# Kernel tuning notes

Measured on AMD Instinct MI355X. Metric: run time of the kernel, lower is better.

Reference implementation:

```python
import jax, jax.numpy as jnp
import numpy as np

B, S, E, H = 4, 2048, 256, 8  # batch, seq_len, embed_dim, depth (heads)


def setup_inputs() -> dict:
    key = jax.random.key(0)
    k_x, k_q, k_k, k_v = jax.random.split(key, 4)
    return {
        "x": jax.random.normal(k_x, (B, S, E), dtype=jnp.float32),
        "w_q": jax.random.normal(k_q, (H, E, E), dtype=jnp.float32),
        "w_k": jax.random.normal(k_k, (H, E, E), dtype=jnp.float32),
        "w_v": jax.random.normal(k_v, (H, E, E), dtype=jnp.float32),
    }


def reference(x, w_q, w_k, w_v):
    # Each head uses full embed_dim projections; heads are averaged at the end.
    embed_dim = x.shape[-1]
    scale = 1.0 / np.sqrt(embed_dim).astype(np.float32)
    q = jnp.einsum("bse,hef->bhsf", x, w_q)  # [B,H,S,E]
    k = jnp.einsum("bse,hef->bhsf", x, w_k)
    v = jnp.einsum("bse,hef->bhsf", x, w_v)
    scores = jax.nn.softmax(jnp.einsum("bhsf,bhtf->bhst", q, k) * scale, axis=-1)
    out = jnp.einsum("bhst,bhtf->bhsf", scores, v)  # [B,H,S,E]
    return out.mean(axis=1)  # [B,S,E]
```

## Files before the change

### kernel.cpp

```cpp
#include <hip/hip_runtime.h>
#include <hip/hip_bf16.h>
#include <cstdint>

#define B_N 4
#define S_N 2048
#define E_N 256
#define H_N 8

typedef float f32x4 __attribute__((ext_vector_type(4)));
typedef int i32x4 __attribute__((ext_vector_type(4)));
typedef short s16x8 __attribute__((ext_vector_type(8)));

static __device__ __forceinline__ f32x4 mfma16(s16x8 a, s16x8 b, f32x4 c) {
  return __builtin_amdgcn_mfma_f32_16x16x32_bf16(a, b, c, 0, 0, 0);
}
static __device__ __forceinline__ i32x4 mfma8i(i32x4 a, i32x4 b, i32x4 c) {
  return __builtin_amdgcn_mfma_i32_16x16x64_i8(a, b, c, 0, 0, 0);
}

static __device__ __forceinline__ unsigned short f2bf(float f) {
  union { float f; unsigned int u; } v; v.f = f;
  unsigned int r = v.u + 0x7fffu + ((v.u >> 16) & 1u);
  return (unsigned short)(r >> 16);
}
static __device__ __forceinline__ float bf2f(unsigned short s) {
  union { unsigned int u; float f; } v; v.u = ((unsigned int)s) << 16;
  return v.f;
}
static __device__ __forceinline__ unsigned short f2bf_fast(float f) {
  __hip_bfloat16 h = __float2bfloat16(f);
  return *(unsigned short*)&h;
}

static __device__ __forceinline__ void limbs(float v, float scale, int& hi8, int& lo8) {
  int x = (int)lrintf(v * scale);
  x = x < -32639 ? -32639 : (x > 32639 ? 32639 : x);
  hi8 = (x + 128) >> 8;
  lo8 = x - (hi8 << 8);
}

static __device__ __forceinline__ void gload16(const void* g, void* l) {
  __builtin_amdgcn_global_load_lds(
      (const __attribute__((address_space(1))) unsigned int*)g,
      (__attribute__((address_space(3))) unsigned int*)l, 16, 0, 0);
}

static __device__ __forceinline__ float dppmax16(float x) {
  x = fmaxf(x, __int_as_float(__builtin_amdgcn_update_dpp(
          0, __float_as_int(x), 0xB1, 0xF, 0xF, true)));
  x = fmaxf(x, __int_as_float(__builtin_amdgcn_update_dpp(
          0, __float_as_int(x), 0x4E, 0xF, 0xF, true)));
  x = fmaxf(x, __int_as_float(__builtin_amdgcn_update_dpp(
          0, __float_as_int(x), 0x141, 0xF, 0xF, true)));
  x = fmaxf(x, __int_as_float(__builtin_amdgcn_update_dpp(
          0, __float_as_int(x), 0x140, 0xF, 0xF, true)));
  return x;
}
static __device__ __forceinline__ float dppsum16(float x) {
  x = x + __int_as_float(__builtin_amdgcn_update_dpp(
          0, __float_as_int(x), 0xB1, 0xF, 0xF, true));
  x = x + __int_as_float(__builtin_amdgcn_update_dpp(
          0, __float_as_int(x), 0x4E, 0xF, 0xF, true));
  x = x + __int_as_float(__builtin_amdgcn_update_dpp(
          0, __float_as_int(x), 0x141, 0xF, 0xF, true));
  x = x + __int_as_float(__builtin_amdgcn_update_dpp(
          0, __float_as_int(x), 0x140, 0xF, 0xF, true));
  return x;
}

__global__ void k_split(const float* __restrict__ src, unsigned short* __restrict__ hi,
                        unsigned short* __restrict__ lo, int n4) {
  int i = blockIdx.x * blockDim.x + threadIdx.x;
  if (i >= n4) return;
  float4 v = ((const float4*)src)[i];
  float f[4] = {v.x, v.y, v.z, v.w};
  unsigned short hh[4], ll[4];
#pragma unroll
  for (int j = 0; j < 4; j++) {
    hh[j] = f2bf(f[j]);
    ll[j] = f2bf(f[j] - bf2f(hh[j]));
  }
  ushort4 h; h.x = hh[0]; h.y = hh[1]; h.z = hh[2]; h.w = hh[3];
  ushort4 l; l.x = ll[0]; l.y = ll[1]; l.z = ll[2]; l.w = ll[3];
  ((ushort4*)hi)[i] = h;
  ((ushort4*)lo)[i] = l;
}

__global__ void k_split8(const float* __restrict__ src, signed char* __restrict__ hi,
                         signed char* __restrict__ lo, int n4) {
  int i = blockIdx.x * blockDim.x + threadIdx.x;
  if (i >= n4) return;
  float4 v = ((const float4*)src)[i];
  float f[4] = {v.x, v.y, v.z, v.w};
  signed char hh[4], ll[4];
#pragma unroll
  for (int j = 0; j < 4; j++) {
    int h8, l8;
    limbs(f[j], 4096.f, h8, l8);
    hh[j] = (signed char)h8;
    ll[j] = (signed char)l8;
  }
  *(int*)(hi + i * 4) = *(int*)hh;
  *(int*)(lo + i * 4) = *(int*)ll;
}

__global__ void k_transpose_wv(const float* __restrict__ wv, unsigned short* __restrict__ wvT) {
  __shared__ float t[32][33];
  int h = blockIdx.z;
  int e0 = blockIdx.x * 32, f0 = blockIdx.y * 32;
  int tx = threadIdx.x & 31, ty = threadIdx.x >> 5;
  const float* src = wv + ((size_t)h * E_N + e0) * E_N + f0;
#pragma unroll
  for (int r = ty; r < 32; r += 8) t[r][tx] = src[(size_t)r * E_N + tx];
  __syncthreads();
  unsigned short* dst = wvT + ((size_t)h * E_N + f0) * E_N + e0;
#pragma unroll
  for (int r = ty; r < 32; r += 8) dst[(size_t)r * E_N + tx] = f2bf(t[tx][r]);
}

#define BKP 40

template <int TERMS, int OUT_MODE>
__global__ __launch_bounds__(256, 2) void k_gemm(
    const unsigned short* __restrict__ Ahi, const unsigned short* __restrict__ Alo,
    const unsigned short* __restrict__ Bhi, const unsigned short* __restrict__ Blo,
    unsigned short* __restrict__ Chi, unsigned short* __restrict__ Clo,
    int K, int N,
    int aDiv, int aMod, long long aStr,
    int bDiv, int bMod, long long bStr,
    long long cStr) {
  __shared__ unsigned short sA[2][128 * BKP];
  __shared__ unsigned short sB[2][128 * BKP];
  int z = blockIdx.z;
  const unsigned short* A0h = Ahi + (long long)((z / aDiv) % aMod) * aStr;
  const unsigned short* A0l = Alo + (long long)((z / aDiv) % aMod) * aStr;
  const unsigned short* B0h = Bhi + (long long)((z / bDiv) % bMod) * bStr;
  const unsigned short* B0l = Blo + (long long)((z / bDiv) % bMod) * bStr;
  int rT = blockIdx.x * 128, cT = blockIdx.y * 128;
  int tid = threadIdx.x;
  int w = tid >> 6, l = tid & 63, lr = l & 15, lg = l >> 4;
  int wr = w >> 1, wc = w & 1;

  f32x4 acc[4][4];
#pragma unroll
  for (int i = 0; i < 4; i++)
#pragma unroll
    for (int j = 0; j < 4; j++) acc[i][j] = (f32x4){0.f, 0.f, 0.f, 0.f};

  for (int k0 = 0; k0 < K; k0 += 32) {
#pragma unroll
    for (int it = 0; it < 2; it++) {
      int idx = (it * 256 + tid) * 8;
      int r = idx >> 5, c = idx & 31;
      *(s16x8*)&sA[0][r * BKP + c] = *(const s16x8*)(A0h + (size_t)(rT + r) * K + k0 + c);
      *(s16x8*)&sB[0][r * BKP + c] = *(const s16x8*)(B0h + (size_t)(cT + r) * K + k0 + c);
      if (TERMS == 3) {
        *(s16x8*)&sA[1][r * BKP + c] = *(const s16x8*)(A0l + (size_t)(rT + r) * K + k0 + c);
        *(s16x8*)&sB[1][r * BKP + c] = *(const s16x8*)(B0l + (size_t)(cT + r) * K + k0 + c);
      }
    }
    __syncthreads();
    s16x8 ah[4], al[4], bh[4], bl[4];
#pragma unroll
    for (int i = 0; i < 4; i++) {
      ah[i] = *(const s16x8*)&sA[0][(wr * 64 + i * 16 + lr) * BKP + lg * 8];
      if (TERMS == 3) al[i] = *(const s16x8*)&sA[1][(wr * 64 + i * 16 + lr) * BKP + lg * 8];
    }
#pragma unroll
    for (int j = 0; j < 4; j++) {
      bh[j] = *(const s16x8*)&sB[0][(wc * 64 + j * 16 + lr) * BKP + lg * 8];
      if (TERMS == 3) bl[j] = *(const s16x8*)&sB[1][(wc * 64 + j * 16 + lr) * BKP + lg * 8];
    }
#pragma unroll
    for (int i = 0; i < 4; i++)
#pragma unroll
      for (int j = 0; j < 4; j++) {
        acc[i][j] = mfma16(ah[i], bh[j], acc[i][j]);
        if (TERMS == 3) {
          acc[i][j] = mfma16(ah[i], bl[j], acc[i][j]);
          acc[i][j] = mfma16(al[i], bh[j], acc[i][j]);
        }
      }
    __syncthreads();
  }
  long long cOff = (long long)z * cStr;
#pragma unroll
  for (int i = 0; i < 4; i++)
#pragma unroll
    for (int j = 0; j < 4; j++)
#pragma unroll
      for (int r = 0; r < 4; r++) {
        int row = rT + wr * 64 + i * 16 + lg * 4 + r;
        int col = cT + wc * 64 + j * 16 + lr;
        float v = acc[i][j][r];
        long long e = cOff + (size_t)row * N + col;
        if (OUT_MODE == 2) {
          int h8, l8;
          limbs(v, 16.f, h8, l8);
          ((signed char*)Chi)[e] = (signed char)h8;
          ((signed char*)Clo)[e] = (signed char)l8;
        } else {
          unsigned short hb = f2bf(v);
          Chi[e] = hb;
          if (OUT_MODE == 1) Clo[e] = f2bf(v - bf2f(hb));
        }
      }
}

#define TT 32
#define BUFS 32768
#define ATTN_LDS 69632
#define THR 40.f

__global__ __launch_bounds__(256, 2) void k_attn(
    const signed char* __restrict__ Y8h, const signed char* __restrict__ Y8l,
    const signed char* __restrict__ X8h, const signed char* __restrict__ X8l,
    const unsigned short* __restrict__ VT, float* __restrict__ Out) {
  extern __shared__ char smem[];

  int obid = blockIdx.x;
  int swz = (obid & 7) * 128 + (obid >> 3);
  int qt = swz & 31, bh = swz >> 5;
  int b = bh >> 3;
  int tid = threadIdx.x, w = tid >> 6, l = tid & 63, lr = l & 15, lg = l >> 4;
  const signed char* Ybh_h = Y8h + (size_t)bh * (S_N * E_N);
  const signed char* Ybh_l = Y8l + (size_t)bh * (S_N * E_N);
  const signed char* Xb_h = X8h + (size_t)b * (S_N * E_N);
  const signed char* Xb_l = X8l + (size_t)b * (S_N * E_N);
  const unsigned short* Vbh = VT + (size_t)bh * (E_N * S_N);
  int qrow = qt * 64 + w * 16;

  int xs8[2];
#pragma unroll
  for (int i = 0; i < 2; i++) {
    int t8 = (w * 2 + i) * 4 + (l >> 4);
    xs8[i] = t8 * 256 + (((l & 15) ^ (t8 & 15)) * 16);
  }
  int vsrc[4];
#pragma unroll
  for (int i = 0; i < 4; i++) {
    int c = (w * 4 + i) * 64 + l;
    vsrc[i] = (c >> 2) * S_N + (c & 3) * 8;
  }

  int xrb[4];
#pragma unroll
  for (int kb = 0; kb < 4; kb++)
    xrb[kb] = lr * 256 + (((kb * 4 + lg) ^ lr) * 16);
  int vtbr = lr * 64 + lg * 16;
  int prb = 65536 + w * 1024 + lr * 64 + ((lg * 16) ^ (((lr >> 2) & 3) << 4));
  int pwb = 65536 + w * 1024 + lg * 256;

  i32x4 yh8[4], yl8[4];
#pragma unroll
  for (int kb = 0; kb < 4; kb++) {
    yh8[kb] = *(const i32x4*)(Ybh_h + (size_t)(qrow + lr) * E_N + kb * 64 + lg * 16);
    yl8[kb] = *(const i32x4*)(Ybh_l + (size_t)(qrow + lr) * E_N + kb * 64 + lg * 16);
  }
  f32x4 o[16];
#pragma unroll
  for (int i = 0; i < 16; i++) o[i] = (f32x4){0.f, 0.f, 0.f, 0.f};
  float m2[4], lv[4];
#pragma unroll
  for (int r = 0; r < 4; r++) { m2[r] = -3.0e38f; lv[r] = 0.f; }

  const float C2T = 1.3758611398590895e-6f;

#pragma unroll
  for (int i = 0; i < 2; i++) {
    gload16(Xb_h + xs8[i], smem + (w * 2 + i) * 1024);
    gload16(Xb_l + xs8[i], smem + 8192 + (w * 2 + i) * 1024);
  }
#pragma unroll
  for (int i = 0; i < 4; i++)
    gload16(Vbh + vsrc[i], smem + 16384 + (w * 4 + i) * 1024);

#define TILE_BODY(CB, NB, t)                                                   \
  {                                                                            \
    asm volatile("s_waitcnt vmcnt(0)" ::: "memory");                           \
    __builtin_amdgcn_s_barrier();                                              \
    if ((t) < 63) {                                                            \
      _Pragma("unroll") for (int i = 0; i < 2; i++) {                          \
        gload16(Xb_h + (size_t)((t) + 1) * (TT * E_N) + xs8[i],                \
                smem + (NB) + (w * 2 + i) * 1024);                             \
        gload16(Xb_l + (size_t)((t) + 1) * (TT * E_N) + xs8[i],                \
                smem + (NB) + 8192 + (w * 2 + i) * 1024);                      \
      }                                                                        \
      _Pragma("unroll") for (int i = 0; i < 4; i++)                            \
          gload16(Vbh + ((t) + 1) * TT + vsrc[i],                              \
                  smem + (NB) + 16384 + (w * 4 + i) * 1024);                   \
    }                                                                          \
    i32x4 i0[2], i1[2], i2[2];                                                 \
    _Pragma("unroll") for (int j = 0; j < 2; j++) {                            \
      i0[j] = (i32x4){0, 0, 0, 0};                                             \
      i1[j] = (i32x4){0, 0, 0, 0};                                             \
      i2[j] = (i32x4){0, 0, 0, 0};                                             \
    }                                                                          \
    __builtin_amdgcn_s_setprio(1);                                             \
    _Pragma("unroll") for (int j = 0; j < 2; j++) {                            \
      _Pragma("unroll") for (int kb = 0; kb < 4; kb++) {                       \
        i32x4 bh_ = *(const i32x4*)(smem + (CB) + j * 4096 + xrb[kb]);         \
        i32x4 bl_ = *(const i32x4*)(smem + (CB) + 8192 + j * 4096 + xrb[kb]);  \
        i0[j] = mfma8i(yh8[kb], bh_, i0[j]);                                   \
        i1[j] = mfma8i(yh8[kb], bl_, i1[j]);                                   \
        i1[j] = mfma8i(yl8[kb], bh_, i1[j]);                                   \
        i2[j] = mfma8i(yl8[kb], bl_, i2[j]);                                   \
      }                                                                        \
    }                                                                          \
    __builtin_amdgcn_s_setprio(0);                                             \
    f32x4 sc[2];                                                               \
    _Pragma("unroll") for (int j = 0; j < 2; j++)                              \
        _Pragma("unroll") for (int r = 0; r < 4; r++)                          \
            sc[j][r] = fmaf(65536.f, (float)i0[j][r],                          \
                            fmaf(256.f, (float)i1[j][r], (float)i2[j][r]));    \
    float t2[4];                                                               \
    _Pragma("unroll") for (int r = 0; r < 4; r++)                              \
        t2[r] = fmaxf(sc[0][r], sc[1][r]) * C2T;                               \
    bool ok = (t2[0] <= m2[0] + THR) && (t2[1] <= m2[1] + THR) &&              \
              (t2[2] <= m2[2] + THR) && (t2[3] <= m2[3] + THR);                \
    if (!__all(ok)) {                                                          \
      float fr[4];                                                             \
      _Pragma("unroll") for (int r = 0; r < 4; r++) {                          \
        float rm = dppmax16(t2[r]);                                            \
        float nm = fmaxf(m2[r], rm);                                           \
        fr[r] = exp2f(m2[r] - nm);                                             \
        m2[r] = nm;                                                            \
        lv[r] *= fr[r];                                                        \
      }                                                                        \
      _Pragma("unroll") for (int i = 0; i < 16; i++)                           \
          _Pragma("unroll") for (int r = 0; r < 4; r++) o[i][r] *= fr[r];      \
    }                                                                          \
    float p[2][4];                                                             \
    _Pragma("unroll") for (int j = 0; j < 2; j++)                              \
        _Pragma("unroll") for (int r = 0; r < 4; r++)                          \
            p[j][r] = exp2f(fmaf(sc[j][r], C2T, -m2[r]));                      \
    _Pragma("unroll") for (int r = 0; r < 4; r++) lv[r] += p[0][r] + p[1][r];  \
    _Pragma("unroll") for (int j = 0; j < 2; j++)                              \
        _Pragma("unroll") for (int r = 0; r < 4; r++) {                        \
      int byt = (32 * j + 2 * lr) ^ (lg << 4);                                 \
      *(unsigned short*)(smem + pwb + r * 64 + byt) = f2bf_fast(p[j][r]);      \
    }                                                                          \
    __builtin_amdgcn_s_setprio(1);                                             \
    {                                                                          \
      int vb = (CB) + 16384 + vtbr;                                            \
      s16x8 pa = *(const s16x8*)(smem + prb);                                  \
      _Pragma("unroll") for (int jf = 0; jf < 16; jf++) {                      \
        s16x8 bv = *(const s16x8*)(smem + vb + jf * 1024);                     \
        o[jf] = mfma16(pa, bv, o[jf]);                                         \
      }                                                                        \
    }                                                                          \
    __builtin_amdgcn_s_setprio(0);                                             \
  }

  for (int kt = 0; kt < S_N / TT; kt += 2) {
    TILE_BODY(0, BUFS, kt);
    TILE_BODY(BUFS, 0, kt + 1);
  }
#undef TILE_BODY

#pragma unroll
  for (int r = 0; r < 4; r++) lv[r] = dppsum16(lv[r]);
#pragma unroll
  for (int jf = 0; jf < 16; jf++)
#pragma unroll
    for (int r = 0; r < 4; r++) {
      float v = o[jf][r] / lv[r] * 0.125f;
      atomicAdd(&Out[((size_t)b * S_N + qrow + lg * 4 + r) * E_N + jf * 16 + lr], v);
    }
}

extern "C" void kernel_launch(void* const* d_in, const int* in_sizes, int n_in,
                              void* d_out, int out_size, void* d_ws, size_t ws_size,
                              hipStream_t stream) {
  const float* x = (const float*)d_in[0];
  const float* wq = (const float*)d_in[1];
  const float* wk = (const float*)d_in[2];
  const float* wv = (const float*)d_in[3];
  float* out = (float*)d_out;

  unsigned short* ws = (unsigned short*)d_ws;
  unsigned short* x_hi = ws;
  unsigned short* x_lo = x_hi + 2097152;
  unsigned short* wq_hi = x_lo + 2097152;
  unsigned short* wq_lo = wq_hi + 524288;
  unsigned short* wk_hi = wq_lo + 524288;
  unsigned short* wk_lo = wk_hi + 524288;
  unsigned short* wvT = wk_lo + 524288;
  unsigned short* mt_hi = wvT + 524288;
  unsigned short* mt_lo = mt_hi + 524288;
  unsigned short* vt = mt_lo + 524288;
  signed char* i8base = (signed char*)(vt + 16777216);
  signed char* y8h = i8base;
  signed char* y8l = y8h + 16777216;
  signed char* x8h = y8l + 16777216;
  signed char* x8l = x8h + 2097152;

  hipMemsetAsync(d_out, 0, (size_t)out_size * sizeof(float), stream);

  k_split<<<2048, 256, 0, stream>>>(x, x_hi, x_lo, 524288);
  k_split<<<512, 256, 0, stream>>>(wq, wq_hi, wq_lo, 131072);
  k_split<<<512, 256, 0, stream>>>(wk, wk_hi, wk_lo, 131072);
  k_split8<<<2048, 256, 0, stream>>>(x, x8h, x8l, 524288);
  k_transpose_wv<<<dim3(8, 8, 8), 256, 0, stream>>>(wv, wvT);

  k_gemm<3, 1><<<dim3(2, 2, 8), 256, 0, stream>>>(
      wk_hi, wk_lo, wq_hi, wq_lo, mt_hi, mt_lo, 256, 256,
      1, 8, 65536LL, 1, 8, 65536LL, 65536LL);
  k_gemm<3, 2><<<dim3(16, 2, 32), 256, 0, stream>>>(
      x_hi, x_lo, mt_hi, mt_lo, (unsigned short*)y8h, (unsigned short*)y8l,
      256, 256, 8, 4, 524288LL, 1, 8, 65536LL, 524288LL);
  k_gemm<1, 0><<<dim3(2, 16, 32), 256, 0, stream>>>(
      wvT, wvT, x_hi, x_hi, vt, vt, 256, 2048,
      1, 8, 65536LL, 8, 4, 524288LL, 524288LL);

  hipFuncSetAttribute((const void*)k_attn, hipFuncAttributeMaxDynamicSharedMemorySize,
                      ATTN_LDS);
  k_attn<<<dim3(1024), 256, ATTN_LDS, stream>>>(y8h, y8l, x8h, x8l, vt, out);
}
```

Measured before the change: 356.5 us.

## Double attention query and key tiles with 512-thread blocks and swizzled V layout

The attention kernel now uses 512-thread blocks covering 128 query rows, and streams 64-key tiles instead of 32. This halves the number of barrier and softmax-rescale iterations and shares each K/V tile load across twice as many waves. The V tile also gets an XOR-swizzled LDS layout to avoid bank conflicts at the wider row stride. In exchange it needs 144KB of LDS per block, so only one block fits per CU. The launch bound of (512,2) may also cap registers tightly enough to cause spills.

Measured after the change: 342.7 us, median of 2. 1.04x faster.

```diff
diff --git a/kernel.cpp b/kernel.cpp
--- a/kernel.cpp
+++ b/kernel.cpp
@@ -207,20 +207,20 @@
       }
 }
 
-#define TT 32
-#define BUFS 32768
-#define ATTN_LDS 69632
+#define TT 64
+#define BUFS 65536
+#define ATTN_LDS 147456
 #define THR 40.f
 
-__global__ __launch_bounds__(256, 2) void k_attn(
+__global__ __launch_bounds__(512, 2) void k_attn(
     const signed char* __restrict__ Y8h, const signed char* __restrict__ Y8l,
     const signed char* __restrict__ X8h, const signed char* __restrict__ X8l,
     const unsigned short* __restrict__ VT, float* __restrict__ Out) {
   extern __shared__ char smem[];
 
   int obid = blockIdx.x;
-  int swz = (obid & 7) * 128 + (obid >> 3);
-  int qt = swz & 31, bh = swz >> 5;
+  int swz = (obid & 7) * 64 + (obid >> 3);
+  int qt = swz & 15, bh = swz >> 4;
   int b = bh >> 3;
   int tid = threadIdx.x, w = tid >> 6, l = tid & 63, lr = l & 15, lg = l >> 4;
   const signed char* Ybh_h = Y8h + (size_t)bh * (S_N * E_N);
@@ -228,28 +228,33 @@
   const signed char* Xb_h = X8h + (size_t)b * (S_N * E_N);
   const signed char* Xb_l = X8l + (size_t)b * (S_N * E_N);
   const unsigned short* Vbh = VT + (size_t)bh * (E_N * S_N);
-  int qrow = qt * 64 + w * 16;
+  int qrow = qt * 128 + w * 16;
 
   int xs8[2];
 #pragma unroll
   for (int i = 0; i < 2; i++) {
-    int t8 = (w * 2 + i) * 4 + (l >> 4);
-    xs8[i] = t8 * 256 + (((l & 15) ^ (t8 & 15)) * 16);
+    int c = (w * 2 + i) * 64 + l;
+    int t8 = c >> 4;
+    xs8[i] = t8 * 256 + (((c & 15) ^ (t8 & 15)) * 16);
   }
   int vsrc[4];
 #pragma unroll
   for (int i = 0; i < 4; i++) {
     int c = (w * 4 + i) * 64 + l;
-    vsrc[i] = (c >> 2) * S_N + (c & 3) * 8;
+    int vrow = c >> 3, vbyt = (c & 7) * 16;
+    vsrc[i] = vrow * S_N + ((vbyt ^ ((vrow & 7) << 4)) >> 1);
   }
 
   int xrb[4];
 #pragma unroll
   for (int kb = 0; kb < 4; kb++)
     xrb[kb] = lr * 256 + (((kb * 4 + lg) ^ lr) * 16);
-  int vtbr = lr * 64 + lg * 16;
-  int prb = 65536 + w * 1024 + lr * 64 + ((lg * 16) ^ (((lr >> 2) & 3) << 4));
-  int pwb = 65536 + w * 1024 + lg * 256;
+  int vtb[2];
+#pragma unroll
+  for (int tc = 0; tc < 2; tc++)
+    vtb[tc] = lr * 128 + ((tc * 64 + lg * 16) ^ ((lr & 7) << 4));
+  int prb = 131072 + w * 2048 + lr * 128 + ((lg * 16) ^ (((lr >> 2) & 3) << 4));
+  int pwb = 131072 + w * 2048 + lg * 512;
 
   i32x4 yh8[4], yl8[4];
 #pragma unroll
@@ -269,53 +274,58 @@
 #pragma unroll
   for (int i = 0; i < 2; i++) {
     gload16(Xb_h + xs8[i], smem + (w * 2 + i) * 1024);
-    gload16(Xb_l + xs8[i], smem + 8192 + (w * 2 + i) * 1024);
+    gload16(Xb_l + xs8[i], smem + 16384 + (w * 2 + i) * 1024);
   }
 #pragma unroll
   for (int i = 0; i < 4; i++)
-    gload16(Vbh + vsrc[i], smem + 16384 + (w * 4 + i) * 1024);
+    gload16(Vbh + vsrc[i], smem + 32768 + (w * 4 + i) * 1024);
 
 #define TILE_BODY(CB, NB, t)                                                   \
   {                                                                            \
     asm volatile("s_waitcnt vmcnt(0)" ::: "memory");                           \
     __builtin_amdgcn_s_barrier();                                              \
-    if ((t) < 63) {                                                            \
+    if ((t) < 31) {                                                            \
       _Pragma("unroll") for (int i = 0; i < 2; i++) {                          \
         gload16(Xb_h + (size_t)((t) + 1) * (TT * E_N) + xs8[i],                \
                 smem + (NB) + (w * 2 + i) * 1024);                             \
         gload16(Xb_l + (size_t)((t) + 1) * (TT * E_N) + xs8[i],                \
-                smem + (NB) + 8192 + (w * 2 + i) * 1024);                      \
+                smem + (NB) + 16384 + (w * 2 + i) * 1024);                     \
       }                                                                        \
       _Pragma("unroll") for (int i = 0; i < 4; i++)                            \
           gload16(Vbh + ((t) + 1) * TT + vsrc[i],                              \
-                  smem + (NB) + 16384 + (w * 4 + i) * 1024);                   \
+                  smem + (NB) + 32768 + (w * 4 + i) * 1024);                   \
     }                                                                          \
-    i32x4 i0[2], i1[2], i2[2];                                                 \
-    _Pragma("unroll") for (int j = 0; j < 2; j++) {                            \
-      i0[j] = (i32x4){0, 0, 0, 0};                                             \
-      i1[j] = (i32x4){0, 0, 0, 0};                                             \
-      i2[j] = (i32x4){0, 0, 0, 0};                                             \
-    }                                                                          \
+    f32x4 sc[4];                                                               \
     __builtin_amdgcn_s_setprio(1);                                             \
-    _Pragma("unroll") for (int j = 0; j < 2; j++) {                            \
-      _Pragma("unroll") for (int kb = 0; kb < 4; kb++) {                       \
-        i32x4 bh_ = *(const i32x4*)(smem + (CB) + j * 4096 + xrb[kb]);         \
-        i32x4 bl_ = *(const i32x4*)(smem + (CB) + 8192 + j * 4096 + xrb[kb]);  \
-        i0[j] = mfma8i(yh8[kb], bh_, i0[j]);                                   \
-        i1[j] = mfma8i(yh8[kb], bl_, i1[j]);                                   \
-        i1[j] = mfma8i(yl8[kb], bh_, i1[j]);                                   \
-        i2[j] = mfma8i(yl8[kb], bl_, i2[j]);                                   \
+    _Pragma("unroll") for (int jp = 0; jp < 4; jp += 2) {                      \
+      i32x4 i0[2], i1[2], i2[2];                                               \
+      _Pragma("unroll") for (int u = 0; u < 2; u++) {                          \
+        i0[u] = (i32x4){0, 0, 0, 0};                                           \
+        i1[u] = (i32x4){0, 0, 0, 0};                                           \
+        i2[u] = (i32x4){0, 0, 0, 0};                                           \
       }                                                                        \
+      _Pragma("unroll") for (int u = 0; u < 2; u++) {                          \
+        _Pragma("unroll") for (int kb = 0; kb < 4; kb++) {                     \
+          i32x4 bh_ = *(const i32x4*)(smem + (CB) + (jp + u) * 4096 + xrb[kb]);\
+          i32x4 bl_ =                                                          \
+              *(const i32x4*)(smem + (CB) + 16384 + (jp + u) * 4096 + xrb[kb]);\
+          i0[u] = mfma8i(yh8[kb], bh_, i0[u]);                                 \
+          i1[u] = mfma8i(yh8[kb], bl_, i1[u]);                                 \
+          i1[u] = mfma8i(yl8[kb], bh_, i1[u]);                                 \
+          i2[u] = mfma8i(yl8[kb], bl_, i2[u]);                                 \
+        }                                                                      \
+      }                                                                        \
+      _Pragma("unroll") for (int u = 0; u < 2; u++)                            \
+          _Pragma("unroll") for (int r = 0; r < 4; r++)                        \
+              sc[jp + u][r] = fmaf(65536.f, (float)i0[u][r],                   \
+                                   fmaf(256.f, (float)i1[u][r],                \
+                                        (float)i2[u][r]));                     \
     }                                                                          \
     __builtin_amdgcn_s_setprio(0);                                             \
-    f32x4 sc[2];                                                               \
-    _Pragma("unroll") for (int j = 0; j < 2; j++)                              \
-        _Pragma("unroll") for (int r = 0; r < 4; r++)                          \
-            sc[j][r] = fmaf(65536.f, (float)i0[j][r],                          \
-                            fmaf(256.f, (float)i1[j][r], (float)i2[j][r]));    \
     float t2[4];                                                               \
     _Pragma("unroll") for (int r = 0; r < 4; r++)                              \
-        t2[r] = fmaxf(sc[0][r], sc[1][r]) * C2T;                               \
+        t2[r] = fmaxf(fmaxf(sc[0][r], sc[1][r]),                               \
+                      fmaxf(sc[2][r], sc[3][r])) * C2T;                        \
     bool ok = (t2[0] <= m2[0] + THR) && (t2[1] <= m2[1] + THR) &&              \
               (t2[2] <= m2[2] + THR) && (t2[3] <= m2[3] + THR);                \
     if (!__all(ok)) {                                                          \
@@ -330,22 +340,23 @@
       _Pragma("unroll") for (int i = 0; i < 16; i++)                           \
           _Pragma("unroll") for (int r = 0; r < 4; r++) o[i][r] *= fr[r];      \
     }                                                                          \
-    float p[2][4];                                                             \
-    _Pragma("unroll") for (int j = 0; j < 2; j++)                              \
+    float p[4][4];                                                             \
+    _Pragma("unroll") for (int j = 0; j < 4; j++)                              \
         _Pragma("unroll") for (int r = 0; r < 4; r++)                          \
             p[j][r] = exp2f(fmaf(sc[j][r], C2T, -m2[r]));                      \
-    _Pragma("unroll") for (int r = 0; r < 4; r++) lv[r] += p[0][r] + p[1][r];  \
-    _Pragma("unroll") for (int j = 0; j < 2; j++)                              \
+    _Pragma("unroll") for (int r = 0; r < 4; r++)                              \
+        lv[r] += (p[0][r] + p[1][r]) + (p[2][r] + p[3][r]);                    \
+    _Pragma("unroll") for (int j = 0; j < 4; j++)                              \
         _Pragma("unroll") for (int r = 0; r < 4; r++) {                        \
       int byt = (32 * j + 2 * lr) ^ (lg << 4);                                 \
-      *(unsigned short*)(smem + pwb + r * 64 + byt) = f2bf_fast(p[j][r]);      \
+      *(unsigned short*)(smem + pwb + r * 128 + byt) = f2bf_fast(p[j][r]);     \
     }                                                                          \
     __builtin_amdgcn_s_setprio(1);                                             \
-    {                                                                          \
-      int vb = (CB) + 16384 + vtbr;                                            \
-      s16x8 pa = *(const s16x8*)(smem + prb);                                  \
+    _Pragma("unroll") for (int tc = 0; tc < 2; tc++) {                         \
+      s16x8 pa = *(const s16x8*)(smem + prb + tc * 64);                        \
       _Pragma("unroll") for (int jf = 0; jf < 16; jf++) {                      \
-        s16x8 bv = *(const s16x8*)(smem + vb + jf * 1024);                     \
+        s16x8 bv =                                                             \
+            *(const s16x8*)(smem + (CB) + 32768 + vtb[tc] + jf * 2048);        \
         o[jf] = mfma16(pa, bv, o[jf]);                                         \
       }                                                                        \
     }                                                                          \
@@ -415,5 +426,5 @@
 
   hipFuncSetAttribute((const void*)k_attn, hipFuncAttributeMaxDynamicSharedMemorySize,
                       ATTN_LDS);
-  k_attn<<<dim3(1024), 256, ATTN_LDS, stream>>>(y8h, y8l, x8h, x8l, vt, out);
-}
+  k_attn<<<dim3(512), 512, ATTN_LDS, stream>>>(y8h, y8l, x8h, x8l, vt, out);
+}
```
